# Kernel tuning notes

Hardware: AMD Instinct MI355X
Metric: run time of the kernel (lower is better)

## Reference

```python
import jax, jax.numpy as jnp
import numpy as np

N = 50000
E = 800000
IN_DIM, HID, OUT = 64, 256, 128


def gcn_conv(x, edge_index, W, b):
    """PyG GCNConv with add_self_loops=False, sym normalization, unit edge weights.
    Transform-then-propagate: out[i] = sum_{e: col[e]=i} norm[e] * (x @ W)[row[e]] + b
    norm[e] = deg^-1/2[row] * deg^-1/2[col], deg = in-degree at col.
    """
    n = x.shape[0]
    row, col = edge_index[0], edge_index[1]
    xw = x @ W  # [N, out]
    deg = jax.ops.segment_sum(jnp.ones(row.shape[0], dtype=x.dtype), col, num_segments=n)
    dis = jnp.where(deg > 0, jax.lax.rsqrt(jnp.where(deg > 0, deg, 1.0)), 0.0)
    norm = dis[row] * dis[col]  # [E]
    msg = xw[row] * norm[:, None]  # [E, out]
    out = jax.ops.segment_sum(msg, col, num_segments=n)
    return out + b


def setup_inputs() -> dict:
    key = jax.random.key(0)
    ks = jax.random.split(key, 16)
    def lin(k, fi, fo):
        s = 1.0 / np.sqrt(fi)
        k1, k2 = jax.random.split(k)
        return (jax.random.uniform(k1, (fi, fo), jnp.float32, -s, s),
                jax.random.uniform(k2, (fo,), jnp.float32, -s, s))
    x = jax.random.normal(ks[0], (N, IN_DIM), jnp.float32)
    edge_index = jax.random.randint(ks[1], (2, E), 0, N, dtype=jnp.int64)
    w_fc, b_fc = lin(ks[2], IN_DIM, HID)
    w_conv1, b_conv1 = lin(ks[3], IN_DIM, HID)
    w_fc1, b_fc1 = lin(ks[4], 2 * HID, OUT)
    w_conv2, b_conv2 = lin(ks[5], 2 * HID, OUT)
    w_fc2, b_fc2 = lin(ks[6], OUT, 1)
    w_conv3, b_conv3 = lin(ks[7], OUT, 1)
    return dict(x=x, edge_index=edge_index,
                w_fc=w_fc, b_fc=b_fc, w_conv1=w_conv1, b_conv1=b_conv1,
                w_fc1=w_fc1, b_fc1=b_fc1, w_conv2=w_conv2, b_conv2=b_conv2,
                w_fc2=w_fc2, b_fc2=b_fc2, w_conv3=w_conv3, b_conv3=b_conv3)


def reference(x, edge_index, w_fc, b_fc, w_conv1, b_conv1, w_fc1, b_fc1,
              w_conv2, b_conv2, w_fc2, b_fc2, w_conv3, b_conv3):
    # MTGCL gcn_mlp, eval mode (dropout / dropout_adj are identity)
    x1 = jax.nn.relu(x @ w_fc + b_fc)                       # [N, HID]
    x2 = jax.nn.relu(gcn_conv(x, edge_index, w_conv1, b_conv1))  # [N, HID]
    x3 = jnp.concatenate((x1, x2), axis=1)                  # [N, 2*HID]
    x5 = jax.nn.relu(x3 @ w_fc1 + b_fc1)                    # [N, OUT]
    x6 = jax.nn.relu(gcn_conv(x3, edge_index, w_conv2, b_conv2))
    x7 = x5 + x6                                            # [N, OUT]
    pre = (x7 @ w_fc2 + b_fc2) + gcn_conv(x7, edge_index, w_conv3, b_conv3)
    return pre  # [N, 1]
```

## Files before the change

### kernel.cpp

```cpp
#include <hip/hip_runtime.h>
#include <hip/hip_bf16.h>

typedef __attribute__((ext_vector_type(8))) short short8;
typedef __attribute__((ext_vector_type(4))) float f32x4;

__device__ __forceinline__ ushort bf16_bits(float v) {
    __hip_bfloat16 h = __float2bfloat16(v);
    return *reinterpret_cast<ushort*>(&h);
}
__device__ __forceinline__ float bf16_val(float v) {
    __hip_bfloat16 h = __float2bfloat16(v);
    return __bfloat162float(h);
}
__device__ __forceinline__ float bfu_lo(uint u) {
    uint t = u << 16; return __uint_as_float(t);
}
__device__ __forceinline__ float bfu_hi(uint u) {
    uint t = u & 0xffff0000u; return __uint_as_float(t);
}


__global__ __launch_bounds__(256) void k_bcount(const int* __restrict__ col,
                                                int* __restrict__ bcnt, int E) {
    __shared__ int hist[196];
    int tid = threadIdx.x;
    int base = blockIdx.x * 2048;
    if (tid < 196) hist[tid] = 0;
    __syncthreads();
    #pragma unroll
    for (int i = 0; i < 8; i++) {
        int e = base + i * 256 + tid;
        if (e < E) atomicAdd(&hist[col[e] >> 8], 1);
    }
    __syncthreads();
    if (tid < 196 && hist[tid] > 0) atomicAdd(&bcnt[tid], hist[tid]);
}

__global__ __launch_bounds__(256) void k_bscan(const int* __restrict__ bcnt,
                                               int* __restrict__ bbase,
                                               int* __restrict__ bcur, int E) {
    int i = threadIdx.x;
    int v = (i < 196) ? bcnt[i] : 0;
    int lane = i & 63, w = i >> 6;
    int s = v;
    #pragma unroll
    for (int o = 1; o < 64; o <<= 1) {
        int t = __shfl_up(s, o);
        if (lane >= o) s += t;
    }
    __shared__ int wsum[4];
    if (lane == 63) wsum[w] = s;
    __syncthreads();
    int add = 0;
    for (int ww = 0; ww < w; ww++) add += wsum[ww];
    int excl = s + add - v;
    if (i < 196) {
        bbase[i] = excl;
        bcur[i] = excl;
    }
    if (i == 195) bbase[196] = excl + v;
}

__global__ __launch_bounds__(256) void k_binA(const int* __restrict__ row,
                                              const int* __restrict__ col,
                                              int* __restrict__ bcur,
                                              uint* __restrict__ stage, int E) {
    __shared__ uint colbuf[2048];
    __shared__ int hist[196];
    __shared__ int lcur[196];
    int tid = threadIdx.x;
    int base = blockIdx.x * 2048;
    if (tid < 196) hist[tid] = 0;
    __syncthreads();
    #pragma unroll
    for (int i = 0; i < 8; i++) {
        int e = base + i * 256 + tid;
        uint c = 0xFFFFFFFFu;
        if (e < E) {
            c = (uint)col[e];
            atomicAdd(&hist[c >> 8], 1);
        }
        colbuf[i * 256 + tid] = c;
    }
    __syncthreads();
    if (tid < 196 && hist[tid] > 0) lcur[tid] = atomicAdd(&bcur[tid], hist[tid]);
    __syncthreads();
    #pragma unroll
    for (int i = 0; i < 8; i++) {
        int idx = i * 256 + tid;
        uint c = colbuf[idx];
        if (c != 0xFFFFFFFFu) {
            uint r = (uint)row[base + idx];
            int p = atomicAdd(&lcur[c >> 8], 1);
            stage[p] = (c << 16) | r;
        }
    }
}

__global__ __launch_bounds__(256) void k_binB(const uint* __restrict__ stage,
                                              const int* __restrict__ bbase,
                                              int* __restrict__ rowptr,
                                              float* __restrict__ dis,
                                              ushort* __restrict__ csr16,
                                              int n, int E) {
    __shared__ int cnt[256];
    __shared__ int cur[256];
    __shared__ int wsum[4];
    int b = blockIdx.x;
    int lo = b << 8;
    int tid = threadIdx.x;
    int gstart = bbase[b], gend = bbase[b + 1];
    cnt[tid] = 0;
    __syncthreads();
    for (int idx = gstart + tid; idx < gend; idx += 256)
        atomicAdd(&cnt[(stage[idx] >> 16) & 255], 1);
    __syncthreads();
    int v = cnt[tid];
    int lane = tid & 63, w = tid >> 6;
    int s = v;
    #pragma unroll
    for (int o = 1; o < 64; o <<= 1) {
        int t = __shfl_up(s, o);
        if (lane >= o) s += t;
    }
    if (lane == 63) wsum[w] = s;
    __syncthreads();
    int add = 0;
    for (int ww = 0; ww < w; ww++) add += wsum[ww];
    int excl = s + add - v + gstart;
    int node = lo + tid;
    if (node < n) {
        rowptr[node] = excl;
        dis[node] = v > 0 ? rsqrtf((float)v) : 0.f;
    }
    cur[tid] = excl;
    if (tid == 0 && b == gridDim.x - 1) rowptr[n] = E;
    __syncthreads();
    for (int idx = gstart + tid; idx < gend; idx += 256) {
        uint pk = stage[idx];
        int p = atomicAdd(&cur[(pk >> 16) & 255], 1);
        csr16[p] = (ushort)(pk & 0xffffu);
    }
}


__global__ __launch_bounds__(256) void k_prepX(const float* __restrict__ x,
                                               const float* __restrict__ dis,
                                               ushort* __restrict__ xh,
                                               ushort* __restrict__ xs, int total4) {
    int i = blockIdx.x * 256 + threadIdx.x;
    if (i >= total4) return;
    float4 v = reinterpret_cast<const float4*>(x)[i];
    float dn = dis[i >> 4];
    float vv[4] = {v.x, v.y, v.z, v.w};
    uint hv[2], sv[2];
    #pragma unroll
    for (int g = 0; g < 2; g++) {
        float a0 = vv[g * 2], a1 = vv[g * 2 + 1];
        hv[g] = (uint)bf16_bits(a0) | ((uint)bf16_bits(a1) << 16);
        sv[g] = (uint)bf16_bits(a0 * dn) | ((uint)bf16_bits(a1 * dn) << 16);
    }
    reinterpret_cast<uint2*>(xh)[i] = make_uint2(hv[0], hv[1]);
    reinterpret_cast<uint2*>(xs)[i] = make_uint2(sv[0], sv[1]);
}


__global__ __launch_bounds__(256) void k_agg64_csr(const ushort* __restrict__ xs,
                                                   const int* __restrict__ rowptr,
                                                   const ushort* __restrict__ csr16,
                                                   const float* __restrict__ dis,
                                                   ushort* __restrict__ agghi, int n) {
    int node = blockIdx.x * 4 + (threadIdx.x >> 6);
    if (node >= n) return;
    int lane = threadIdx.x & 63;
    int sub = lane >> 3;
    int li  = lane & 7;
    int s = rowptr[node], t = rowptr[node + 1];
    float acc[8] = {};
    int p = s;
    for (; p + 16 <= t; p += 16) {
        int rr[2];
        #pragma unroll
        for (int u = 0; u < 2; u++) rr[u] = csr16[p + u * 8 + sub];
        uint4 v[2];
        #pragma unroll
        for (int u = 0; u < 2; u++)
            v[u] = *reinterpret_cast<const uint4*>(&xs[(size_t)rr[u] * 64 + li * 8]);
        #pragma unroll
        for (int u = 0; u < 2; u++) {
            acc[0] += bfu_lo(v[u].x); acc[1] += bfu_hi(v[u].x);
            acc[2] += bfu_lo(v[u].y); acc[3] += bfu_hi(v[u].y);
            acc[4] += bfu_lo(v[u].z); acc[5] += bfu_hi(v[u].z);
            acc[6] += bfu_lo(v[u].w); acc[7] += bfu_hi(v[u].w);
        }
    }
    for (; p < t; p += 8) {
        int e = p + sub;
        if (e < t) {
            int rr = csr16[e];
            uint4 v = *reinterpret_cast<const uint4*>(&xs[(size_t)rr * 64 + li * 8]);
            acc[0] += bfu_lo(v.x); acc[1] += bfu_hi(v.x);
            acc[2] += bfu_lo(v.y); acc[3] += bfu_hi(v.y);
            acc[4] += bfu_lo(v.z); acc[5] += bfu_hi(v.z);
            acc[6] += bfu_lo(v.w); acc[7] += bfu_hi(v.w);
        }
    }
    #pragma unroll
    for (int j = 0; j < 8; j++) {
        acc[j] += __shfl_xor(acc[j], 8);
        acc[j] += __shfl_xor(acc[j], 16);
        acc[j] += __shfl_xor(acc[j], 32);
    }
    if (sub == 0) {
        float dn = dis[node];
        uint hp[4];
        #pragma unroll
        for (int g = 0; g < 4; g++) {
            float a0 = acc[g * 2] * dn, a1 = acc[g * 2 + 1] * dn;
            hp[g] = (uint)bf16_bits(a0) | ((uint)bf16_bits(a1) << 16);
        }
        *reinterpret_cast<uint4*>(&agghi[(size_t)node * 64 + li * 8]) =
            make_uint4(hp[0], hp[1], hp[2], hp[3]);
    }
}

__global__ __launch_bounds__(256) void k_agg128_x7dot(
    const ushort* __restrict__ xw,
    const int* __restrict__ rowptr,
    const ushort* __restrict__ csr16,
    const float* __restrict__ dis,
    const float* __restrict__ b2,
    const ushort* __restrict__ x5,
    const float* __restrict__ wfc2, const float* __restrict__ bfc2,
    const float* __restrict__ wc3,  const float* __restrict__ bc3,
    float* __restrict__ out, float* __restrict__ xw3, int n) {
    int node = blockIdx.x * 4 + (threadIdx.x >> 6);
    if (node >= n) return;
    int lane = threadIdx.x & 63;
    int sub = lane >> 4;
    int li  = lane & 15;
    int s = rowptr[node], t = rowptr[node + 1];
    float acc[8] = {};
    int p = s;
    for (; p + 16 <= t; p += 16) {
        int rr[4];
        #pragma unroll
        for (int u = 0; u < 4; u++) rr[u] = csr16[p + u * 4 + sub];
        uint4 v[4];
        #pragma unroll
        for (int u = 0; u < 4; u++)
            v[u] = *reinterpret_cast<const uint4*>(&xw[(size_t)rr[u] * 128 + li * 8]);
        #pragma unroll
        for (int u = 0; u < 4; u++) {
            acc[0] += bfu_lo(v[u].x); acc[1] += bfu_hi(v[u].x);
            acc[2] += bfu_lo(v[u].y); acc[3] += bfu_hi(v[u].y);
            acc[4] += bfu_lo(v[u].z); acc[5] += bfu_hi(v[u].z);
            acc[6] += bfu_lo(v[u].w); acc[7] += bfu_hi(v[u].w);
        }
    }
    for (; p < t; p += 4) {
        int e = p + sub;
        if (e < t) {
            int rr = csr16[e];
            uint4 v = *reinterpret_cast<const uint4*>(&xw[(size_t)rr * 128 + li * 8]);
            acc[0] += bfu_lo(v.x); acc[1] += bfu_hi(v.x);
            acc[2] += bfu_lo(v.y); acc[3] += bfu_hi(v.y);
            acc[4] += bfu_lo(v.z); acc[5] += bfu_hi(v.z);
            acc[6] += bfu_lo(v.w); acc[7] += bfu_hi(v.w);
        }
    }
    #pragma unroll
    for (int j = 0; j < 8; j++) {
        acc[j] += __shfl_xor(acc[j], 16);
        acc[j] += __shfl_xor(acc[j], 32);
    }
    float dn = dis[node];
    float s1 = 0.f, s2 = 0.f;
    if (sub == 0) {
        uint4 xv = *reinterpret_cast<const uint4*>(&x5[(size_t)node * 128 + li * 8]);
        float xr[8] = {bfu_lo(xv.x), bfu_hi(xv.x), bfu_lo(xv.y), bfu_hi(xv.y),
                       bfu_lo(xv.z), bfu_hi(xv.z), bfu_lo(xv.w), bfu_hi(xv.w)};
        #pragma unroll
        for (int j = 0; j < 8; j++) {
            int d = li * 8 + j;
            float x7 = xr[j] + fmaxf(dn * acc[j] + b2[d], 0.f);
            s1 += x7 * wfc2[d];
            s2 += x7 * wc3[d];
        }
    }
    #pragma unroll
    for (int o = 32; o > 0; o >>= 1) {
        s1 += __shfl_down(s1, o);
        s2 += __shfl_down(s2, o);
    }
    if (lane == 0) {
        out[node] = s1 + bfc2[0] + bc3[0];
        xw3[node] = s2 * dn;
    }
}

__global__ __launch_bounds__(256) void k_agg1_csr(const float* __restrict__ sv,
                                                  const int* __restrict__ rowptr,
                                                  const ushort* __restrict__ csr16,
                                                  const float* __restrict__ dis,
                                                  float* __restrict__ out, int n) {
    int i = blockIdx.x * 256 + threadIdx.x;
    if (i >= n) return;
    int s = rowptr[i], t = rowptr[i + 1];
    float a = 0.f;
    #pragma unroll 4
    for (int p = s; p < t; ++p) a += sv[csr16[p]];
    out[i] += dis[i] * a;
}

__global__ __launch_bounds__(256) void k_prepW(const float* __restrict__ w0,
                                               const float* __restrict__ w1,
                                               const float* __restrict__ wf1,
                                               const float* __restrict__ wf2,
                                               ushort* __restrict__ W0f,
                                               ushort* __restrict__ W1f,
                                               ushort* __restrict__ Bf) {
    int id = blockIdx.x * 256 + threadIdx.x;
    if (id < 8192) {
        int mat = id >> 12;
        int rem = id & 4095;
        int lane = rem & 63;
        int nt = (rem >> 6) & 15;
        int k0i = (rem >> 10) & 1;
        int arr = rem >> 11;
        const float* w = mat ? w1 : w0;
        ushort* dst = mat ? W1f : W0f;
        int n = nt * 16 + (lane & 15);
        int kb = k0i * 32 + (lane >> 4) * 8;
        ushort o[8];
        #pragma unroll
        for (int j = 0; j < 8; j++) {
            float v = w[(size_t)(kb + j) * 256 + n];
            o[j] = arr ? bf16_bits(v - bf16_val(v)) : bf16_bits(v);
        }
        *reinterpret_cast<int4*>(&dst[(size_t)rem * 8]) = *reinterpret_cast<const int4*>(o);
    } else if (id < 24576) {
        int rem = id - 8192;
        int lane = rem & 63;
        int nt   = (rem >> 6) & 15;
        int k0i  = (rem >> 10) & 15;
        int n = nt * 16 + (lane & 15);
        int kbase = k0i * 32 + (lane >> 4) * 8;
        ushort outv[8];
        #pragma unroll
        for (int j = 0; j < 8; j++) {
            int k = kbase + j;
            float v = (n < 128) ? wf1[(size_t)k * 128 + n]
                                : wf2[(size_t)k * 128 + (n - 128)];
            outv[j] = bf16_bits(v);
        }
        *reinterpret_cast<int4*>(&Bf[(size_t)rem * 8]) = *reinterpret_cast<const int4*>(outv);
    }
}

__device__ __forceinline__ int x3_swz(int inner) {
    return inner ^ ((((inner >> 6) & 1) << 4) ^ (((inner >> 7) & 1) << 3));
}

__global__ __launch_bounds__(512) void k_mmfused(
    const ushort* __restrict__ xh, const ushort* __restrict__ ah_,
    const ushort* __restrict__ W0f, const ushort* __restrict__ W1f,
    const float* __restrict__ b0, const float* __restrict__ b1,
    const ushort* __restrict__ Bf, const float* __restrict__ bias1,
    const float* __restrict__ dis,
    ushort* __restrict__ C1, ushort* __restrict__ C2, int M) {
    __shared__ ushort x3[4 * 16 * 512];

    const int t = threadIdx.x;
    const int lane = t & 63;
    const int wv = t >> 6;
    const int m0 = blockIdx.x * 64;
    const int ln15 = lane & 15;
    const int quad = lane >> 4;

    f32x4 acc[4][2];

    #pragma unroll
    for (int layer = 0; layer < 2; layer++) {
        const ushort* A = layer ? ah_ : xh;
        const ushort* Wf = layer ? W1f : W0f;
        const float* bias = layer ? b1 : b0;
        #pragma unroll
        for (int mt = 0; mt < 4; mt++)
            #pragma unroll
            for (int ntl = 0; ntl < 2; ntl++)
                acc[mt][ntl] = (f32x4){0.f, 0.f, 0.f, 0.f};

        short8 wh[2][2], wl[2][2], av[2][4];
        #pragma unroll
        for (int k0i = 0; k0i < 2; k0i++) {
            #pragma unroll
            for (int ntl = 0; ntl < 2; ntl++) {
                const ushort* pw = Wf + ((size_t)k0i * 16 + wv * 2 + ntl) * 512 + (size_t)lane * 8;
                wh[k0i][ntl] = *reinterpret_cast<const short8*>(pw);
                wl[k0i][ntl] = *reinterpret_cast<const short8*>(pw + 16384);
            }
            #pragma unroll
            for (int mt = 0; mt < 4; mt++) {
                int gm = m0 + mt * 16 + ln15;
                int gmc = gm < M - 1 ? gm : M - 1;
                size_t ia = (size_t)gmc * 64 + k0i * 32 + quad * 8;
                av[k0i][mt] = *reinterpret_cast<const short8*>(&A[ia]);
            }
        }
        #pragma unroll
        for (int k0i = 0; k0i < 2; k0i++) {
            #pragma unroll
            for (int mt = 0; mt < 4; mt++) {
                #pragma unroll
                for (int ntl = 0; ntl < 2; ntl++)
                    acc[mt][ntl] = __builtin_amdgcn_mfma_f32_16x16x32_bf16(av[k0i][mt], wh[k0i][ntl], acc[mt][ntl], 0, 0, 0);
                #pragma unroll
                for (int ntl = 0; ntl < 2; ntl++)
                    acc[mt][ntl] = __builtin_amdgcn_mfma_f32_16x16x32_bf16(av[k0i][mt], wl[k0i][ntl], acc[mt][ntl], 0, 0, 0);
            }
        }

        #pragma unroll
        for (int mt = 0; mt < 4; mt++) {
            #pragma unroll
            for (int ntl = 0; ntl < 2; ntl++) {
                int gn = (wv * 2 + ntl) * 16 + ln15;
                int gcol = gn + layer * 256;
                int k0f = gcol >> 5, qf = (gcol >> 3) & 3, j = gcol & 7;
                #pragma unroll
                for (int r = 0; r < 4; r++) {
                    int rloc = quad * 4 + r;
                    float v = fmaxf(acc[mt][ntl][r] + bias[gn], 0.f);
                    int inner = x3_swz((qf * 16 + rloc) * 8 + j);
                    x3[(mt * 16 + k0f) * 512 + inner] = bf16_bits(v);
                }
            }
        }
    }
    __syncthreads();

    #pragma unroll
    for (int mt = 0; mt < 4; mt++)
        #pragma unroll
        for (int ntl = 0; ntl < 2; ntl++)
            acc[mt][ntl] = (f32x4){0.f, 0.f, 0.f, 0.f};

    const int innerA = x3_swz(lane * 8);
    const ushort* bPtr = Bf + ((size_t)wv * 2) * 512 + (size_t)lane * 8;

    auto ldB = [&](int k0, short8* dst) {
        #pragma unroll
        for (int ntl = 0; ntl < 2; ntl++)
            dst[ntl] = *reinterpret_cast<const short8*>(bPtr + ((size_t)k0 * 16 + ntl) * 512);
    };
    auto ldA = [&](int k0, short8* dst) {
        #pragma unroll
        for (int mt = 0; mt < 4; mt++)
            dst[mt] = *reinterpret_cast<const short8*>(&x3[(mt * 16 + k0) * 512 + innerA]);
    };

    short8 b0r[2], b1r[2], b2r[2], b3r[2];
    short8 aC[4], aN[4];
    ldB(0, b0r); ldB(1, b1r); ldB(2, b2r); ldB(3, b3r);
    ldA(0, aC);

    #pragma unroll
    for (int k4 = 0; k4 < 4; k4++) {
        #pragma unroll
        for (int j = 0; j < 4; j++) {
            const int k0 = k4 * 4 + j;
            short8* bcur = (j == 0) ? b0r : (j == 1) ? b1r : (j == 2) ? b2r : b3r;
            short8 tB[2];
            int kpre = k0 + 4 < 16 ? k0 + 4 : 0;
            ldB(kpre, tB);
            int ka = k0 + 1 < 16 ? k0 + 1 : 0;
            ldA(ka, aN);
            #pragma unroll
            for (int mt = 0; mt < 4; mt++)
                #pragma unroll
                for (int ntl = 0; ntl < 2; ntl++)
                    acc[mt][ntl] = __builtin_amdgcn_mfma_f32_16x16x32_bf16(aC[mt], bcur[ntl], acc[mt][ntl], 0, 0, 0);
            bcur[0] = tB[0]; bcur[1] = tB[1];
            #pragma unroll
            for (int mt = 0; mt < 4; mt++) aC[mt] = aN[mt];
        }
    }
    __syncthreads();

    #pragma unroll
    for (int mt = 0; mt < 4; mt++) {
        float dn[4];
        #pragma unroll
        for (int r = 0; r < 4; r++) {
            int gm = m0 + mt * 16 + quad * 4 + r;
            dn[r] = (gm < M) ? dis[gm] : 0.f;
        }
        #pragma unroll
        for (int ntl = 0; ntl < 2; ntl++) {
            int gn = (wv * 2 + ntl) * 16 + ln15;
            #pragma unroll
            for (int r = 0; r < 4; r++) {
                int row64 = mt * 16 + quad * 4 + r;
                float v = acc[mt][ntl][r];
                ushort ov = (gn < 128) ? bf16_bits(fmaxf(v + bias1[gn], 0.f))
                                       : bf16_bits(v * dn[r]);
                int idx = row64 * 256 + gn;
                idx ^= ((row64 >> 2) & 3) << 4;
                x3[idx] = ov;
            }
        }
    }
    __syncthreads();

    #pragma unroll
    for (int c = 0; c < 4; c++) {
        int offu = c * 4096 + t * 8;
        int row64 = offu >> 8;
        int colu = offu & 255;
        int src = row64 * 256 + (colu ^ (((row64 >> 2) & 3) << 4));
        uint4 v = *reinterpret_cast<const uint4*>(&x3[src]);
        int gm = m0 + row64;
        if (gm < M) {
            if (colu < 128)
                *reinterpret_cast<uint4*>(&C1[(size_t)gm * 128 + colu]) = v;
            else
                *reinterpret_cast<uint4*>(&C2[(size_t)gm * 128 + (colu - 128)]) = v;
        }
    }
}

extern "C" void kernel_launch(void* const* d_in, const int* in_sizes, int n_in,
                              void* d_out, int out_size, void* d_ws, size_t ws_size,
                              hipStream_t stream) {
    const float* x       = (const float*)d_in[0];
    const int*   ei      = (const int*)d_in[1];
    const float* w_fc    = (const float*)d_in[2];
    const float* b_fc    = (const float*)d_in[3];
    const float* w_conv1 = (const float*)d_in[4];
    const float* b_conv1 = (const float*)d_in[5];
    const float* w_fc1   = (const float*)d_in[6];
    const float* b_fc1   = (const float*)d_in[7];
    const float* w_conv2 = (const float*)d_in[8];
    const float* b_conv2 = (const float*)d_in[9];
    const float* w_fc2   = (const float*)d_in[10];
    const float* b_fc2   = (const float*)d_in[11];
    const float* w_conv3 = (const float*)d_in[12];
    const float* b_conv3 = (const float*)d_in[13];

    const int N = in_sizes[0] / 64;
    const int E = in_sizes[1] / 2;
    const int* row = ei;
    const int* col = ei + E;

    const int nb = (N + 255) / 256;
    const int nblk = (N + 63) / 64;

    char* p = (char*)d_ws;
    auto alloc = [&](size_t elems) {
        void* q = p; p += ((elems + 3) & ~(size_t)3) * 4; return q;
    };
    int*    bcnt    = (int*)   alloc(200);
    int*    bbase   = (int*)   alloc(200);
    int*    bcur    = (int*)   alloc(200);
    int*    rowptr  = (int*)   alloc(N + 4);
    uint*   stage   = (uint*)  alloc(E);
    ushort* csr16   = (ushort*)alloc((size_t)E / 2);
    float*  dis     = (float*) alloc(N);
    ushort* xh      = (ushort*)alloc((size_t)N * 32);
    ushort* xs      = (ushort*)alloc((size_t)N * 32);
    ushort* agghi   = (ushort*)alloc((size_t)N * 32);
    ushort* Bf      = (ushort*)alloc(65536);
    ushort* W0f     = (ushort*)alloc(16384);
    ushort* W1f     = (ushort*)alloc(16384);
    ushort* x5      = (ushort*)alloc((size_t)N * 64);
    ushort* xw2     = (ushort*)alloc((size_t)N * 64);
    float*  xw3     = (float*) alloc(N);

    float* out = (float*)d_out;

    hipMemsetAsync(bcnt, 0, 196 * sizeof(int), stream);
    k_bcount<<<(E + 2047) / 2048, 256, 0, stream>>>(col, bcnt, E);
    k_bscan<<<1, 256, 0, stream>>>(bcnt, bbase, bcur, E);
    k_binA<<<(E + 2047) / 2048, 256, 0, stream>>>(row, col, bcur, stage, E);
    k_binB<<<nb, 256, 0, stream>>>(stage, bbase, rowptr, dis, csr16, N, E);

    k_prepX<<<(N * 16 + 255) / 256, 256, 0, stream>>>(x, dis, xh, xs, N * 16);
    k_prepW<<<24576 / 256, 256, 0, stream>>>(w_fc, w_conv1, w_fc1, w_conv2,
                                             W0f, W1f, Bf);

    k_agg64_csr<<<(N + 3) / 4, 256, 0, stream>>>(xs, rowptr, csr16, dis, agghi, N);

    k_mmfused<<<nblk, 512, 0, stream>>>(xh, agghi, W0f, W1f, b_fc, b_conv1,
                                        Bf, b_fc1, dis, x5, xw2, N);

    k_agg128_x7dot<<<(N + 3) / 4, 256, 0, stream>>>(
        xw2, rowptr, csr16, dis, b_conv2, x5,
        w_fc2, b_fc2, w_conv3, b_conv3, out, xw3, N);

    k_agg1_csr<<<(N + 255) / 256, 256, 0, stream>>>(xw3, rowptr, csr16, dis, out, N);
}
```

Baseline: 242.4 us.

## Hand-schedule global loads with inline asm and explicit vmcnt waits in fused matmul

Replaces compiler-generated loads in the fused matmul kernel with inline global_load_dwordx4 plus explicit s_waitcnt vmcnt counters and sched barriers. The second layer's operand loads are issued before the first layer's epilogue, and the B-operand prefetch in the second GEMM becomes a four-deep ring with precise wait counts. The goal is to overlap global memory latency with MFMA and epilogue work. The cost is fragile hand-tuned waitcnt values, more live registers, and sched barriers that limit the compiler's own reordering.

```diff
diff --git a/kernel.cpp b/kernel.cpp
--- a/kernel.cpp
+++ b/kernel.cpp
@@ -3,6 +3,7 @@
 
 typedef __attribute__((ext_vector_type(8))) short short8;
 typedef __attribute__((ext_vector_type(4))) float f32x4;
+typedef __attribute__((ext_vector_type(4))) uint uint4e;
 
 __device__ __forceinline__ ushort bf16_bits(float v) {
     __hip_bfloat16 h = __float2bfloat16(v);
@@ -17,6 +18,11 @@
 }
 __device__ __forceinline__ float bfu_hi(uint u) {
     uint t = u & 0xffff0000u; return __uint_as_float(t);
+}
+
+__device__ __forceinline__ void gload16(uint4e& d, const ushort* p) {
+    asm volatile("global_load_dwordx4 %0, %1, off"
+                 : "=&v"(d) : "v"(p) : "memory");
 }
 
 
@@ -380,47 +386,47 @@
 
     f32x4 acc[4][2];
 
-    #pragma unroll
-    for (int layer = 0; layer < 2; layer++) {
-        const ushort* A = layer ? ah_ : xh;
-        const ushort* Wf = layer ? W1f : W0f;
-        const float* bias = layer ? b1 : b0;
-        #pragma unroll
-        for (int mt = 0; mt < 4; mt++)
-            #pragma unroll
-            for (int ntl = 0; ntl < 2; ntl++)
-                acc[mt][ntl] = (f32x4){0.f, 0.f, 0.f, 0.f};
-
-        short8 wh[2][2], wl[2][2], av[2][4];
+    auto issueLayer = [&](const ushort* A, const ushort* Wf,
+                          uint4e (&wS)[8], uint4e (&aS)[8]) {
         #pragma unroll
         for (int k0i = 0; k0i < 2; k0i++) {
             #pragma unroll
             for (int ntl = 0; ntl < 2; ntl++) {
                 const ushort* pw = Wf + ((size_t)k0i * 16 + wv * 2 + ntl) * 512 + (size_t)lane * 8;
-                wh[k0i][ntl] = *reinterpret_cast<const short8*>(pw);
-                wl[k0i][ntl] = *reinterpret_cast<const short8*>(pw + 16384);
+                gload16(wS[k0i * 4 + ntl * 2 + 0], pw);
+                gload16(wS[k0i * 4 + ntl * 2 + 1], pw + 16384);
             }
             #pragma unroll
             for (int mt = 0; mt < 4; mt++) {
                 int gm = m0 + mt * 16 + ln15;
                 int gmc = gm < M - 1 ? gm : M - 1;
-                size_t ia = (size_t)gmc * 64 + k0i * 32 + quad * 8;
-                av[k0i][mt] = *reinterpret_cast<const short8*>(&A[ia]);
+                gload16(aS[k0i * 4 + mt], &A[(size_t)gmc * 64 + k0i * 32 + quad * 8]);
             }
         }
+    };
+    auto mfmaLayer = [&](uint4e (&wS)[8], uint4e (&aS)[8]) {
+        #pragma unroll
+        for (int mt = 0; mt < 4; mt++)
+            #pragma unroll
+            for (int ntl = 0; ntl < 2; ntl++)
+                acc[mt][ntl] = (f32x4){0.f, 0.f, 0.f, 0.f};
         #pragma unroll
         for (int k0i = 0; k0i < 2; k0i++) {
             #pragma unroll
             for (int mt = 0; mt < 4; mt++) {
+                short8 a = __builtin_bit_cast(short8, aS[k0i * 4 + mt]);
                 #pragma unroll
                 for (int ntl = 0; ntl < 2; ntl++)
-                    acc[mt][ntl] = __builtin_amdgcn_mfma_f32_16x16x32_bf16(av[k0i][mt], wh[k0i][ntl], acc[mt][ntl], 0, 0, 0);
+                    acc[mt][ntl] = __builtin_amdgcn_mfma_f32_16x16x32_bf16(
+                        a, __builtin_bit_cast(short8, wS[k0i * 4 + ntl * 2 + 0]), acc[mt][ntl], 0, 0, 0);
                 #pragma unroll
                 for (int ntl = 0; ntl < 2; ntl++)
-                    acc[mt][ntl] = __builtin_amdgcn_mfma_f32_16x16x32_bf16(av[k0i][mt], wl[k0i][ntl], acc[mt][ntl], 0, 0, 0);
+                    acc[mt][ntl] = __builtin_amdgcn_mfma_f32_16x16x32_bf16(
+                        a, __builtin_bit_cast(short8, wS[k0i * 4 + ntl * 2 + 1]), acc[mt][ntl], 0, 0, 0);
             }
         }
-
+    };
+    auto epiLayer = [&](const float* bias, int layer) {
         #pragma unroll
         for (int mt = 0; mt < 4; mt++) {
             #pragma unroll
@@ -437,6 +443,20 @@
                 }
             }
         }
+    };
+
+    {
+        uint4e wS0[8], aS0[8], wS1[8], aS1[8];
+        issueLayer(xh, W0f, wS0, aS0);
+        asm volatile("s_waitcnt vmcnt(0)" ::: "memory");
+        __builtin_amdgcn_sched_barrier(0);
+        mfmaLayer(wS0, aS0);
+        issueLayer(ah_, W1f, wS1, aS1);
+        epiLayer(b0, 0);
+        asm volatile("s_waitcnt vmcnt(0)" ::: "memory");
+        __builtin_amdgcn_sched_barrier(0);
+        mfmaLayer(wS1, aS1);
+        epiLayer(b1, 1);
     }
     __syncthreads();
 
@@ -449,43 +469,47 @@
     const int innerA = x3_swz(lane * 8);
     const ushort* bPtr = Bf + ((size_t)wv * 2) * 512 + (size_t)lane * 8;
 
-    auto ldB = [&](int k0, short8* dst) {
-        #pragma unroll
-        for (int ntl = 0; ntl < 2; ntl++)
-            dst[ntl] = *reinterpret_cast<const short8*>(bPtr + ((size_t)k0 * 16 + ntl) * 512);
-    };
     auto ldA = [&](int k0, short8* dst) {
         #pragma unroll
         for (int mt = 0; mt < 4; mt++)
             dst[mt] = *reinterpret_cast<const short8*>(&x3[(mt * 16 + k0) * 512 + innerA]);
     };
 
-    short8 b0r[2], b1r[2], b2r[2], b3r[2];
+    uint4e bb[4][2];
     short8 aC[4], aN[4];
-    ldB(0, b0r); ldB(1, b1r); ldB(2, b2r); ldB(3, b3r);
+
+#define ISSUE_B(K0) { \
+    gload16(bb[(K0) & 3][0], bPtr + ((size_t)(K0) * 16 + 0) * 512); \
+    gload16(bb[(K0) & 3][1], bPtr + ((size_t)(K0) * 16 + 1) * 512); }
+
+#define P2_STEP(K0, VMSTR) { \
+    if ((K0) < 15) ldA((K0) + 1, aN); \
+    asm volatile("s_waitcnt " VMSTR ::: "memory"); \
+    __builtin_amdgcn_sched_barrier(0); \
+    short8 bc0 = __builtin_bit_cast(short8, bb[(K0) & 3][0]); \
+    short8 bc1 = __builtin_bit_cast(short8, bb[(K0) & 3][1]); \
+    _Pragma("unroll") \
+    for (int mt = 0; mt < 4; mt++) { \
+        acc[mt][0] = __builtin_amdgcn_mfma_f32_16x16x32_bf16(aC[mt], bc0, acc[mt][0], 0, 0, 0); \
+        acc[mt][1] = __builtin_amdgcn_mfma_f32_16x16x32_bf16(aC[mt], bc1, acc[mt][1], 0, 0, 0); \
+    } \
+    if ((K0) < 12) ISSUE_B((K0) + 4); \
+    _Pragma("unroll") \
+    for (int mt = 0; mt < 4; mt++) aC[mt] = aN[mt]; }
+
+    ISSUE_B(0); ISSUE_B(1); ISSUE_B(2); ISSUE_B(3);
     ldA(0, aC);
-
-    #pragma unroll
-    for (int k4 = 0; k4 < 4; k4++) {
-        #pragma unroll
-        for (int j = 0; j < 4; j++) {
-            const int k0 = k4 * 4 + j;
-            short8* bcur = (j == 0) ? b0r : (j == 1) ? b1r : (j == 2) ? b2r : b3r;
-            short8 tB[2];
-            int kpre = k0 + 4 < 16 ? k0 + 4 : 0;
-            ldB(kpre, tB);
-            int ka = k0 + 1 < 16 ? k0 + 1 : 0;
-            ldA(ka, aN);
-            #pragma unroll
-            for (int mt = 0; mt < 4; mt++)
-                #pragma unroll
-                for (int ntl = 0; ntl < 2; ntl++)
-                    acc[mt][ntl] = __builtin_amdgcn_mfma_f32_16x16x32_bf16(aC[mt], bcur[ntl], acc[mt][ntl], 0, 0, 0);
-            bcur[0] = tB[0]; bcur[1] = tB[1];
-            #pragma unroll
-            for (int mt = 0; mt < 4; mt++) aC[mt] = aN[mt];
-        }
-    }
+    P2_STEP(0,  "vmcnt(6)");  P2_STEP(1,  "vmcnt(6)");
+    P2_STEP(2,  "vmcnt(6)");  P2_STEP(3,  "vmcnt(6)");
+    P2_STEP(4,  "vmcnt(6)");  P2_STEP(5,  "vmcnt(6)");
+    P2_STEP(6,  "vmcnt(6)");  P2_STEP(7,  "vmcnt(6)");
+    P2_STEP(8,  "vmcnt(6)");  P2_STEP(9,  "vmcnt(6)");
+    P2_STEP(10, "vmcnt(6)");  P2_STEP(11, "vmcnt(6)");
+    P2_STEP(12, "vmcnt(6)");  P2_STEP(13, "vmcnt(4)");
+    P2_STEP(14, "vmcnt(2)");  P2_STEP(15, "vmcnt(0)");
+#undef P2_STEP
+#undef ISSUE_B
+
     __syncthreads();
 
     #pragma unroll
```

Result: slower. 254.3 us (+4.9%).
